# Kernel optimization log

Measured on AMD Instinct MI355X. Metric: run time of the kernel, lower is better.

## Reference

```python
import jax, jax.numpy as jnp
import numpy as np

NEG_INF = -1e9  # matches masked_fill value -1000000000.0
LEAKY_SLOPE = 0.2


def setup_inputs() -> dict:
    key = jax.random.key(0)
    k1, k2, k3, k4 = jax.random.split(key, 4)
    B, N, D_in, D_out = 8, 2048, 256, 256
    x = jax.random.normal(k1, (B, N, D_in), dtype=jnp.float32)
    adj_matrix = jax.random.randint(k2, (B, N, N), 0, 2, dtype=jnp.int32)
    # torch nn.Linear weights: W is [out, in], attention a is [1, 2*out]
    W = jax.random.normal(k3, (D_out, D_in), dtype=jnp.float32) / np.sqrt(D_in)
    a = jax.random.normal(k4, (1, 2 * D_out), dtype=jnp.float32) / np.sqrt(2 * D_out)
    return {"x": x, "adj_matrix": adj_matrix, "W": W, "a": a}


def reference(x, adj_matrix, W, a):
    # h = W(x): [B, N, D_out]
    h = jnp.einsum('bnd,od->bno', x, W)
    D = h.shape[-1]
    # attention(concat(h_i, h_j)) == h_i @ a_left + h_j @ a_right (bias-free linear)
    a_left, a_right = a[0, :D], a[0, D:]
    e = (h @ a_left)[:, :, None] + (h @ a_right)[:, None, :]  # [B, N, N]
    e = jnp.where(e > 0, e, LEAKY_SLOPE * e)  # LeakyReLU(0.2)
    e = jnp.where(adj_matrix == 0, NEG_INF, e)
    alpha = jax.nn.softmax(e, axis=-1)
    return jnp.einsum('bij,bjd->bid', alpha, h)
```

## Files before the change

kernel.cpp:

```cpp
#include <hip/hip_runtime.h>
#include <hip/hip_bf16.h>

typedef __attribute__((ext_vector_type(8))) __bf16 bf16x8;
typedef __attribute__((ext_vector_type(4))) float f32x4;
typedef __attribute__((ext_vector_type(4))) int int4v;

#define NB 8
#define NN 2048
#define ND 256
#define L2E 1.44269504f
#define AS1 __attribute__((address_space(1)))
#define AS3 __attribute__((address_space(3)))

__global__ __launch_bounds__(256) void k2_elr(
    const float* __restrict__ x, const float* __restrict__ W,
    const float* __restrict__ a, float* __restrict__ elc,
    float* __restrict__ er2) {
  __shared__ float wls[ND], wrs[ND];
  int t = threadIdx.x;
  {
    float swl = 0.f, swr = 0.f;
    for (int o = 0; o < ND; ++o) {
      float wv = W[(long)o * ND + t];
      swl = fmaf(a[o], wv, swl);
      swr = fmaf(a[ND + o], wv, swr);
    }
    wls[t] = swl;
    wrs[t] = swr;
  }
  __syncthreads();
  int r = t >> 2, q = t & 3;
  long row = (long)blockIdx.x * 64 + r;
  const f32x4* xr = (const f32x4*)(x + row * ND);
  float sl = 0.f, sr = 0.f;
#pragma unroll
  for (int ii = 0; ii < 16; ++ii) {
    int idx = q + (ii << 2);
    f32x4 xv = xr[idx];
    f32x4 lv = *(const f32x4*)(wls + idx * 4);
    f32x4 rv = *(const f32x4*)(wrs + idx * 4);
    sl += xv[0] * lv[0] + xv[1] * lv[1] + xv[2] * lv[2] + xv[3] * lv[3];
    sr += xv[0] * rv[0] + xv[1] * rv[1] + xv[2] * rv[2] + xv[3] * rv[3];
  }
  sl += __shfl_xor(sl, 1);
  sl += __shfl_xor(sl, 2);
  sr += __shfl_xor(sr, 1);
  sr += __shfl_xor(sr, 2);
  if (q == 0) {
    elc[row] = (-0.8f * sl - 16.0f) * L2E;
    float2 v;
    v.x = (sr - 16.0f) * L2E;
    v.y = 0.2f * sr * L2E;
    *(float2*)(er2 + row * 2) = v;
  }
}

__global__ __launch_bounds__(256) void k1_h(
    const float* __restrict__ x, const float* __restrict__ W,
    __bf16* __restrict__ hT2) {
  __shared__ __bf16 hlds[256 * 34];
  int tid = threadIdx.x;
  int wid = tid >> 6, lane = tid & 63;
  int msub = wid & 1, nh = wid >> 1;
  int lrow = lane & 15, kg = lane >> 4;
  int m0 = blockIdx.x * 32;
  int row = m0 + msub * 16 + lrow;

  f32x4 acc[8];
#pragma unroll
  for (int f = 0; f < 8; ++f) acc[f] = (f32x4){0.f, 0.f, 0.f, 0.f};

#pragma unroll
  for (int k0 = 0; k0 < ND; k0 += 32) {
    int kk = k0 + kg * 8;
    const f32x4* xa = (const f32x4*)(x + (long)row * ND + kk);
    f32x4 a0 = xa[0], a1 = xa[1];
    bf16x8 afrag;
    afrag[0] = (__bf16)a0[0]; afrag[1] = (__bf16)a0[1];
    afrag[2] = (__bf16)a0[2]; afrag[3] = (__bf16)a0[3];
    afrag[4] = (__bf16)a1[0]; afrag[5] = (__bf16)a1[1];
    afrag[6] = (__bf16)a1[2]; afrag[7] = (__bf16)a1[3];
#pragma unroll
    for (int f = 0; f < 8; ++f) {
      int o = nh * 128 + f * 16 + lrow;
      const f32x4* wb = (const f32x4*)(W + (long)o * ND + kk);
      f32x4 b0 = wb[0], b1 = wb[1];
      bf16x8 bfrag;
      bfrag[0] = (__bf16)b0[0]; bfrag[1] = (__bf16)b0[1];
      bfrag[2] = (__bf16)b0[2]; bfrag[3] = (__bf16)b0[3];
      bfrag[4] = (__bf16)b1[0]; bfrag[5] = (__bf16)b1[1];
      bfrag[6] = (__bf16)b1[2]; bfrag[7] = (__bf16)b1[3];
      acc[f] = __builtin_amdgcn_mfma_f32_16x16x32_bf16(afrag, bfrag, acc[f], 0, 0, 0);
    }
  }

#pragma unroll
  for (int f = 0; f < 8; ++f) {
    int d = nh * 128 + f * 16 + lrow;
#pragma unroll
    for (int r = 0; r < 4; ++r) {
      int nloc = msub * 16 + kg * 4 + r;
      hlds[d * 34 + nloc] = (__bf16)acc[f][r];
    }
  }
  __syncthreads();
  {
    int b = m0 >> 11;
    int jc = (m0 & (NN - 1)) >> 5;
    const int* src = (const int*)(hlds + tid * 34);
    int tmp[16];
#pragma unroll
    for (int j = 0; j < 16; ++j) tmp[j] = src[j];
    __bf16* dst = hT2 + (((long)b * 64 + jc) * 256 + tid) * 32;
#pragma unroll
    for (int j = 0; j < 4; ++j)
      *(int4v*)(dst + j * 8) = *(int4v*)(tmp + j * 4);
  }
}

__global__ __launch_bounds__(512, 4) void k3_main(
    const int* __restrict__ adj, const __bf16* __restrict__ hT2,
    const float* __restrict__ elc, const float* __restrict__ er2,
    float* __restrict__ out) {
  __shared__ __bf16 hbuf[4][8192];
  __shared__ float er_lds[NN * 2];

  int blk = blockIdx.x;
  int b = blk & 7;
  int it = blk >> 3;
  int tid = threadIdx.x;
  int wid = tid >> 6, lane = tid & 63;
  int isub = wid & 1, dh = wid >> 1;
  int lrow = lane & 15, kg = lane >> 4;
  int irow = it * 32 + isub * 16 + lrow;

  const __bf16* hT2b = hT2 + (long)b * 64 * 8192;
  const int* adjrow = adj + ((long)b * NN + irow) * NN;
  const float* er2b = er2 + (long)b * NN * 2;
  float c1s = elc[b * NN + irow];
  int kg8 = kg * 8;

  __builtin_amdgcn_global_load_lds((const AS1 void*)(er2b + tid * 4),
                                   (AS3 void*)(er_lds + tid * 4), 16, 0, 0);
  __builtin_amdgcn_global_load_lds((const AS1 void*)(er2b + 2048 + tid * 4),
                                   (AS3 void*)(er_lds + 2048 + tid * 4), 16, 0, 0);

  int d0 = tid >> 2, slot = tid & 3;
  int jlog = slot ^ (d0 & 3) ^ ((d0 >> 2) & 3);
  const __bf16* sgbase = hT2b + d0 * 32 + jlog * 8;

  int slot_r = kg ^ (lrow & 3) ^ ((lrow >> 2) & 3);
  int hoff = (dh * 64 + lrow) * 64 + slot_r * 16;
  int d_base = dh * 64 + lrow;

  f32x4 acc[4];
#pragma unroll
  for (int f = 0; f < 4; ++f) acc[f] = (f32x4){0.f, 0.f, 0.f, 0.f};
  float den = 0.f;

  int4v aj0_0, aj1_0, aj0_1, aj1_1, aj0_2, aj1_2, aj0_3, aj1_3;

#define STAGEH(BI, TCV)                                                     \
  {                                                                         \
    const __bf16* s_ = sgbase + (long)(TCV)*8192;                           \
    __builtin_amdgcn_global_load_lds((const AS1 void*)(s_),                 \
                                     (AS3 void*)(&hbuf[BI][tid * 8]), 16, 0, 0); \
    __builtin_amdgcn_global_load_lds(                                       \
        (const AS1 void*)(s_ + 4096),                                       \
        (AS3 void*)(&hbuf[BI][4096 + tid * 8]), 16, 0, 0);                  \
  }

#define LOADADJ(S, TCV)                                                     \
  {                                                                         \
    const int* ap_ = adjrow + (TCV)*32 + kg8;                               \
    aj0_##S = *(const int4v*)(ap_);                                         \
    aj1_##S = *(const int4v*)(ap_ + 4);                                     \
  }

#define COMPUTE(BI, S, TCV)                                                 \
  {                                                                         \
    const float* ep_ = er_lds + ((TCV)*32 + kg8) * 2;                       \
    f32x4 e0 = *(const f32x4*)(ep_);                                        \
    f32x4 e1 = *(const f32x4*)(ep_ + 4);                                    \
    f32x4 e2 = *(const f32x4*)(ep_ + 8);                                    \
    f32x4 e3 = *(const f32x4*)(ep_ + 12);                                   \
    bf16x8 pfrag;                                                           \
    float ps = 0.f;                                                         \
    _Pragma("unroll") for (int e = 0; e < 8; ++e) {                         \
      f32x4 ev = (e < 2) ? e0 : (e < 4) ? e1 : (e < 6) ? e2 : e3;           \
      float x16 = ev[(e & 1) * 2];                                          \
      float x02 = ev[(e & 1) * 2 + 1];                                      \
      int aj = (e < 4) ? aj0_##S[e] : aj1_##S[e & 3];                       \
      float m = fmaxf(x16, x02 + c1s);                                      \
      float p = __builtin_amdgcn_exp2f(m);                                  \
      p = aj ? p : 0.0f;                                                    \
      ps += p;                                                              \
      pfrag[e] = (__bf16)p;                                                 \
    }                                                                       \
    den += ps;                                                              \
    const char* hb = (const char*)&hbuf[BI][0];                             \
    __builtin_amdgcn_s_setprio(1);                                          \
    _Pragma("unroll") for (int f = 0; f < 4; ++f) {                         \
      bf16x8 bfr = *(const bf16x8*)(hb + hoff + f * 1024);                  \
      acc[f] = __builtin_amdgcn_mfma_f32_16x16x32_bf16(pfrag, bfr, acc[f], 0, 0, 0); \
    }                                                                       \
    __builtin_amdgcn_s_setprio(0);                                          \
  }

#define WAITB(VMN)                                       \
  asm volatile("s_waitcnt vmcnt(" VMN ")" ::: "memory"); \
  __builtin_amdgcn_s_barrier();

  LOADADJ(0, 0); STAGEH(0, 0);
  LOADADJ(1, 1); STAGEH(1, 1);
  LOADADJ(2, 2); STAGEH(2, 2);

  for (int t4 = 0; t4 < 15; ++t4) {
    int tc = t4 * 4;
    WAITB("8"); STAGEH(3, tc + 3); LOADADJ(3, tc + 3); COMPUTE(0, 0, tc);
    WAITB("8"); STAGEH(0, tc + 4); LOADADJ(0, tc + 4); COMPUTE(1, 1, tc + 1);
    WAITB("8"); STAGEH(1, tc + 5); LOADADJ(1, tc + 5); COMPUTE(2, 2, tc + 2);
    WAITB("8"); STAGEH(2, tc + 6); LOADADJ(2, tc + 6); COMPUTE(3, 3, tc + 3);
  }
  WAITB("8"); STAGEH(3, 63); LOADADJ(3, 63); COMPUTE(0, 0, 60);
  WAITB("8"); COMPUTE(1, 1, 61);
  WAITB("4"); COMPUTE(2, 2, 62);
  WAITB("0"); COMPUTE(3, 3, 63);

#undef STAGEH
#undef LOADADJ
#undef COMPUTE
#undef WAITB

  den += __shfl_xor(den, 16);
  den += __shfl_xor(den, 32);
  float rdiv[4];
#pragma unroll
  for (int r = 0; r < 4; ++r) rdiv[r] = 1.0f / __shfl(den, kg * 4 + r);

  float* outb = out + ((long)b * NN + it * 32 + isub * 16) * ND;
#pragma unroll
  for (int f = 0; f < 4; ++f) {
    int dcol = d_base + f * 16;
#pragma unroll
    for (int r = 0; r < 4; ++r)
      outb[(long)(kg * 4 + r) * ND + dcol] = acc[f][r] * rdiv[r];
  }
}

extern "C" void kernel_launch(void* const* d_in, const int* in_sizes, int n_in,
                              void* d_out, int out_size, void* d_ws,
                              size_t ws_size, hipStream_t stream) {
  const float* x = (const float*)d_in[0];
  const int* adj = (const int*)d_in[1];
  const float* W = (const float*)d_in[2];
  const float* a = (const float*)d_in[3];
  float* out = (float*)d_out;

  char* ws = (char*)d_ws;
  const size_t base = 8u * 1024u * 1024u;
  __bf16* hT2 = (__bf16*)ws;
  float* elc = (float*)(ws + base);
  float* er2 = (float*)(ws + base + 65536u);

  k1_h<<<dim3(512), dim3(256), 0, stream>>>(x, W, hT2);
  k2_elr<<<dim3(256), dim3(256), 0, stream>>>(x, W, a, elc, er2);
  k3_main<<<dim3(512), dim3(512), 0, stream>>>(adj, hT2, elc, er2, out);
}
```

Before: 131.8 us.

## Pack adjacency into bitmask in a pre-pass and shrink main-loop staging

Adds a pre-pass kernel that turns the int32 adjacency matrix into 64-bit ballot bitmasks. The main kernel then loads each block's 32-row mask slice into LDS once instead of streaming int adjacency per tile. The main loop drops from four h buffers to three, with a simpler swizzle and wait counts. The pre-pass still reads the full 128MB adjacency, so the main kernel's saving is traded for an extra full pass plus a launch.

Measured after the change: 131.7 us. About the same (-0.1%).

```diff
diff --git a/kernel.cpp b/kernel.cpp
--- a/kernel.cpp
+++ b/kernel.cpp
@@ -11,6 +11,19 @@
 #define L2E 1.44269504f
 #define AS1 __attribute__((address_space(1)))
 #define AS3 __attribute__((address_space(3)))
+
+__global__ __launch_bounds__(256) void k5_pack(
+    const int* __restrict__ adj, unsigned long long* __restrict__ mask) {
+  const long NSEG = (long)NB * NN * (NN / 64);
+  int lane = threadIdx.x & 63;
+  long gw = (((long)blockIdx.x * 256 + threadIdx.x) >> 6);
+  long stride = ((long)gridDim.x * 256) >> 6;
+  for (long s = gw; s < NSEG; s += stride) {
+    int v = adj[s * 64 + lane];
+    unsigned long long m = __ballot(v != 0);
+    if (lane == 0) mask[s] = m;
+  }
+}
 
 __global__ __launch_bounds__(256) void k2_elr(
     const float* __restrict__ x, const float* __restrict__ W,
@@ -119,11 +132,12 @@
 }
 
 __global__ __launch_bounds__(512, 4) void k3_main(
-    const int* __restrict__ adj, const __bf16* __restrict__ hT2,
+    const unsigned* __restrict__ mask32, const __bf16* __restrict__ hT2,
     const float* __restrict__ elc, const float* __restrict__ er2,
     float* __restrict__ out) {
-  __shared__ __bf16 hbuf[4][8192];
+  __shared__ __bf16 hbuf[3][8192];
   __shared__ float er_lds[NN * 2];
+  __shared__ unsigned mask_lds[32 * 65];
 
   int blk = blockIdx.x;
   int b = blk & 7;
@@ -135,100 +149,97 @@
   int irow = it * 32 + isub * 16 + lrow;
 
   const __bf16* hT2b = hT2 + (long)b * 64 * 8192;
-  const int* adjrow = adj + ((long)b * NN + irow) * NN;
+  const unsigned* maskb = mask32 + ((long)b * NN + (long)it * 32) * 64;
   const float* er2b = er2 + (long)b * NN * 2;
   float c1s = elc[b * NN + irow];
   int kg8 = kg * 8;
 
+  int4v mw = *(const int4v*)(maskb + tid * 4);
   __builtin_amdgcn_global_load_lds((const AS1 void*)(er2b + tid * 4),
                                    (AS3 void*)(er_lds + tid * 4), 16, 0, 0);
   __builtin_amdgcn_global_load_lds((const AS1 void*)(er2b + 2048 + tid * 4),
                                    (AS3 void*)(er_lds + 2048 + tid * 4), 16, 0, 0);
 
   int d0 = tid >> 2, slot = tid & 3;
-  int jlog = slot ^ (d0 & 3) ^ ((d0 >> 2) & 3);
+  int jlog = slot ^ ((d0 >> 1) & 3);
   const __bf16* sgbase = hT2b + d0 * 32 + jlog * 8;
 
-  int slot_r = kg ^ (lrow & 3) ^ ((lrow >> 2) & 3);
-  int hoff = (dh * 64 + lrow) * 64 + slot_r * 16;
+#define STAGEH(BI, TCV)                                                      \
+  {                                                                          \
+    const __bf16* s_ = sgbase + (long)(TCV)*8192;                            \
+    __builtin_amdgcn_global_load_lds((const AS1 void*)(s_),                  \
+                                     (AS3 void*)(&hbuf[BI][tid * 8]), 16, 0, 0); \
+    __builtin_amdgcn_global_load_lds(                                        \
+        (const AS1 void*)(s_ + 4096),                                        \
+        (AS3 void*)(&hbuf[BI][4096 + tid * 8]), 16, 0, 0);                   \
+  }
+
+  STAGEH(0, 0);
+  STAGEH(1, 1);
+
+  asm volatile("s_waitcnt vmcnt(6)" ::: "memory");
+  {
+    int mrow = tid >> 4, mcol = (tid & 15) * 4;
+    *(int4v*)(mask_lds + mrow * 65 + mcol) = mw;
+  }
+  asm volatile("s_waitcnt lgkmcnt(0)" ::: "memory");
+  __builtin_amdgcn_s_barrier();
+
+  int hoff = (dh * 64 + lrow) * 64 + (kg ^ ((lrow >> 1) & 3)) * 16;
   int d_base = dh * 64 + lrow;
+  int mbase = (isub * 16 + lrow) * 65;
 
   f32x4 acc[4];
 #pragma unroll
   for (int f = 0; f < 4; ++f) acc[f] = (f32x4){0.f, 0.f, 0.f, 0.f};
   float den = 0.f;
 
-  int4v aj0_0, aj1_0, aj0_1, aj1_1, aj0_2, aj1_2, aj0_3, aj1_3;
-
-#define STAGEH(BI, TCV)                                                     \
-  {                                                                         \
-    const __bf16* s_ = sgbase + (long)(TCV)*8192;                           \
-    __builtin_amdgcn_global_load_lds((const AS1 void*)(s_),                 \
-                                     (AS3 void*)(&hbuf[BI][tid * 8]), 16, 0, 0); \
-    __builtin_amdgcn_global_load_lds(                                       \
-        (const AS1 void*)(s_ + 4096),                                       \
-        (AS3 void*)(&hbuf[BI][4096 + tid * 8]), 16, 0, 0);                  \
-  }
-
-#define LOADADJ(S, TCV)                                                     \
-  {                                                                         \
-    const int* ap_ = adjrow + (TCV)*32 + kg8;                               \
-    aj0_##S = *(const int4v*)(ap_);                                         \
-    aj1_##S = *(const int4v*)(ap_ + 4);                                     \
-  }
-
-#define COMPUTE(BI, S, TCV)                                                 \
-  {                                                                         \
-    const float* ep_ = er_lds + ((TCV)*32 + kg8) * 2;                       \
-    f32x4 e0 = *(const f32x4*)(ep_);                                        \
-    f32x4 e1 = *(const f32x4*)(ep_ + 4);                                    \
-    f32x4 e2 = *(const f32x4*)(ep_ + 8);                                    \
-    f32x4 e3 = *(const f32x4*)(ep_ + 12);                                   \
-    bf16x8 pfrag;                                                           \
-    float ps = 0.f;                                                         \
-    _Pragma("unroll") for (int e = 0; e < 8; ++e) {                         \
-      f32x4 ev = (e < 2) ? e0 : (e < 4) ? e1 : (e < 6) ? e2 : e3;           \
-      float x16 = ev[(e & 1) * 2];                                          \
-      float x02 = ev[(e & 1) * 2 + 1];                                      \
-      int aj = (e < 4) ? aj0_##S[e] : aj1_##S[e & 3];                       \
-      float m = fmaxf(x16, x02 + c1s);                                      \
-      float p = __builtin_amdgcn_exp2f(m);                                  \
-      p = aj ? p : 0.0f;                                                    \
-      ps += p;                                                              \
-      pfrag[e] = (__bf16)p;                                                 \
-    }                                                                       \
-    den += ps;                                                              \
-    const char* hb = (const char*)&hbuf[BI][0];                             \
-    __builtin_amdgcn_s_setprio(1);                                          \
-    _Pragma("unroll") for (int f = 0; f < 4; ++f) {                         \
-      bf16x8 bfr = *(const bf16x8*)(hb + hoff + f * 1024);                  \
+#define COMPUTE(BI, TCV)                                                     \
+  {                                                                          \
+    unsigned msh = mask_lds[mbase + (TCV)] >> kg8;                           \
+    const float* ep_ = er_lds + ((TCV)*32 + kg8) * 2;                        \
+    f32x4 e0 = *(const f32x4*)(ep_);                                         \
+    f32x4 e1 = *(const f32x4*)(ep_ + 4);                                     \
+    f32x4 e2 = *(const f32x4*)(ep_ + 8);                                     \
+    f32x4 e3 = *(const f32x4*)(ep_ + 12);                                    \
+    bf16x8 pfrag;                                                            \
+    float ps = 0.f;                                                          \
+    _Pragma("unroll") for (int e = 0; e < 8; ++e) {                          \
+      f32x4 ev = (e < 2) ? e0 : (e < 4) ? e1 : (e < 6) ? e2 : e3;            \
+      float x16 = ev[(e & 1) * 2];                                           \
+      float x02 = ev[(e & 1) * 2 + 1];                                       \
+      float m = fmaxf(x16, x02 + c1s);                                       \
+      float p = __builtin_amdgcn_exp2f(m);                                   \
+      p = ((msh >> e) & 1u) ? p : 0.0f;                                      \
+      ps += p;                                                               \
+      pfrag[e] = (__bf16)p;                                                  \
+    }                                                                        \
+    den += ps;                                                               \
+    const char* hb = (const char*)&hbuf[BI][0];                              \
+    __builtin_amdgcn_s_setprio(1);                                           \
+    _Pragma("unroll") for (int f = 0; f < 4; ++f) {                          \
+      bf16x8 bfr = *(const bf16x8*)(hb + hoff + f * 1024);                   \
       acc[f] = __builtin_amdgcn_mfma_f32_16x16x32_bf16(pfrag, bfr, acc[f], 0, 0, 0); \
-    }                                                                       \
-    __builtin_amdgcn_s_setprio(0);                                          \
+    }                                                                        \
+    __builtin_amdgcn_s_setprio(0);                                           \
   }
 
 #define WAITB(VMN)                                       \
   asm volatile("s_waitcnt vmcnt(" VMN ")" ::: "memory"); \
   __builtin_amdgcn_s_barrier();
 
-  LOADADJ(0, 0); STAGEH(0, 0);
-  LOADADJ(1, 1); STAGEH(1, 1);
-  LOADADJ(2, 2); STAGEH(2, 2);
-
-  for (int t4 = 0; t4 < 15; ++t4) {
-    int tc = t4 * 4;
-    WAITB("8"); STAGEH(3, tc + 3); LOADADJ(3, tc + 3); COMPUTE(0, 0, tc);
-    WAITB("8"); STAGEH(0, tc + 4); LOADADJ(0, tc + 4); COMPUTE(1, 1, tc + 1);
-    WAITB("8"); STAGEH(1, tc + 5); LOADADJ(1, tc + 5); COMPUTE(2, 2, tc + 2);
-    WAITB("8"); STAGEH(2, tc + 6); LOADADJ(2, tc + 6); COMPUTE(3, 3, tc + 3);
-  }
-  WAITB("8"); STAGEH(3, 63); LOADADJ(3, 63); COMPUTE(0, 0, 60);
-  WAITB("8"); COMPUTE(1, 1, 61);
-  WAITB("4"); COMPUTE(2, 2, 62);
-  WAITB("0"); COMPUTE(3, 3, 63);
+  for (int t3 = 0; t3 < 20; ++t3) {
+    int tc = t3 * 3;
+    WAITB("2"); STAGEH(2, tc + 2); COMPUTE(0, tc);
+    WAITB("2"); STAGEH(0, tc + 3); COMPUTE(1, tc + 1);
+    WAITB("2"); STAGEH(1, tc + 4); COMPUTE(2, tc + 2);
+  }
+  WAITB("2"); STAGEH(2, 62); COMPUTE(0, 60);
+  WAITB("2"); STAGEH(0, 63); COMPUTE(1, 61);
+  WAITB("2"); COMPUTE(2, 62);
+  WAITB("0"); COMPUTE(0, 63);
 
 #undef STAGEH
-#undef LOADADJ
 #undef COMPUTE
 #undef WAITB
 
@@ -262,8 +273,12 @@
   __bf16* hT2 = (__bf16*)ws;
   float* elc = (float*)(ws + base);
   float* er2 = (float*)(ws + base + 65536u);
-
+  unsigned long long* mask =
+      (unsigned long long*)(ws + base + 262144u);
+
+  k5_pack<<<dim3(2048), dim3(256), 0, stream>>>(adj, mask);
   k1_h<<<dim3(512), dim3(256), 0, stream>>>(x, W, hT2);
   k2_elr<<<dim3(256), dim3(256), 0, stream>>>(x, W, a, elc, er2);
-  k3_main<<<dim3(512), dim3(512), 0, stream>>>(adj, hT2, elc, er2, out);
-}
+  k3_main<<<dim3(512), dim3(512), 0, stream>>>((const unsigned*)mask, hT2, elc,
+                                               er2, out);
+}
```

## Compress adjacency to LDS bitmasks via ballot and reuse h fragments across rows

Applied to the files above, without the earlier changes.

The main kernel is restructured to 256 threads per block. Each wave now owns 64 output columns for all 32 rows, so every h fragment read from LDS feeds two MFMAs. Adjacency rows are loaded coalesced along j, turned into 64-bit masks with a wave ballot, and stored as bit masks in LDS, replacing the per-lane int4 adjacency registers. The second right-attention term is now recomputed with an FMA from the first, which halves the er array. The trade-offs are extra LDS traffic and barriers for the mask handoff, a deeper software pipeline, and more registers per thread for the doubled accumulators.

Measured after the change: 125.5 us. -4.8%, faster.

```diff
diff --git a/kernel.cpp b/kernel.cpp
--- a/kernel.cpp
+++ b/kernel.cpp
@@ -15,7 +15,7 @@
 __global__ __launch_bounds__(256) void k2_elr(
     const float* __restrict__ x, const float* __restrict__ W,
     const float* __restrict__ a, float* __restrict__ elc,
-    float* __restrict__ er2) {
+    float* __restrict__ erx) {
   __shared__ float wls[ND], wrs[ND];
   int t = threadIdx.x;
   {
@@ -48,10 +48,7 @@
   sr += __shfl_xor(sr, 2);
   if (q == 0) {
     elc[row] = (-0.8f * sl - 16.0f) * L2E;
-    float2 v;
-    v.x = (sr - 16.0f) * L2E;
-    v.y = 0.2f * sr * L2E;
-    *(float2*)(er2 + row * 2) = v;
+    erx[row] = (sr - 16.0f) * L2E;
   }
 }
 
@@ -118,133 +115,170 @@
   }
 }
 
-__global__ __launch_bounds__(512, 4) void k3_main(
+__global__ __launch_bounds__(256, 2) void k3_main(
     const int* __restrict__ adj, const __bf16* __restrict__ hT2,
-    const float* __restrict__ elc, const float* __restrict__ er2,
+    const float* __restrict__ elc, const float* __restrict__ erx,
     float* __restrict__ out) {
   __shared__ __bf16 hbuf[4][8192];
-  __shared__ float er_lds[NN * 2];
+  __shared__ float er_lds[NN];
+  __shared__ unsigned mask_lds[2048];
 
   int blk = blockIdx.x;
   int b = blk & 7;
   int it = blk >> 3;
   int tid = threadIdx.x;
   int wid = tid >> 6, lane = tid & 63;
-  int isub = wid & 1, dh = wid >> 1;
   int lrow = lane & 15, kg = lane >> 4;
-  int irow = it * 32 + isub * 16 + lrow;
+  int kg8 = kg * 8;
 
   const __bf16* hT2b = hT2 + (long)b * 64 * 8192;
-  const int* adjrow = adj + ((long)b * NN + irow) * NN;
-  const float* er2b = er2 + (long)b * NN * 2;
-  float c1s = elc[b * NN + irow];
-  int kg8 = kg * 8;
-
-  __builtin_amdgcn_global_load_lds((const AS1 void*)(er2b + tid * 4),
+  const int* adjb = adj + ((long)b * NN + (long)it * 32) * NN;
+  const int* adjw = adjb + (long)wid * 8 * NN;
+  const float* erxb = erx + (long)b * NN;
+
+  float c1s0 = elc[b * NN + it * 32 + lrow];
+  float c1s1 = elc[b * NN + it * 32 + 16 + lrow];
+
+  __builtin_amdgcn_global_load_lds((const AS1 void*)(erxb + tid * 4),
                                    (AS3 void*)(er_lds + tid * 4), 16, 0, 0);
-  __builtin_amdgcn_global_load_lds((const AS1 void*)(er2b + 2048 + tid * 4),
-                                   (AS3 void*)(er_lds + 2048 + tid * 4), 16, 0, 0);
+  __builtin_amdgcn_global_load_lds((const AS1 void*)(erxb + 1024 + tid * 4),
+                                   (AS3 void*)(er_lds + 1024 + tid * 4), 16, 0, 0);
 
   int d0 = tid >> 2, slot = tid & 3;
-  int jlog = slot ^ (d0 & 3) ^ ((d0 >> 2) & 3);
+  int jlog = slot ^ ((tid >> 3) & 3);
   const __bf16* sgbase = hT2b + d0 * 32 + jlog * 8;
 
-  int slot_r = kg ^ (lrow & 3) ^ ((lrow >> 2) & 3);
-  int hoff = (dh * 64 + lrow) * 64 + slot_r * 16;
-  int d_base = dh * 64 + lrow;
-
-  f32x4 acc[4];
-#pragma unroll
-  for (int f = 0; f < 4; ++f) acc[f] = (f32x4){0.f, 0.f, 0.f, 0.f};
-  float den = 0.f;
-
-  int4v aj0_0, aj1_0, aj0_1, aj1_1, aj0_2, aj1_2, aj0_3, aj1_3;
-
-#define STAGEH(BI, TCV)                                                     \
-  {                                                                         \
-    const __bf16* s_ = sgbase + (long)(TCV)*8192;                           \
-    __builtin_amdgcn_global_load_lds((const AS1 void*)(s_),                 \
-                                     (AS3 void*)(&hbuf[BI][tid * 8]), 16, 0, 0); \
-    __builtin_amdgcn_global_load_lds(                                       \
-        (const AS1 void*)(s_ + 4096),                                       \
-        (AS3 void*)(&hbuf[BI][4096 + tid * 8]), 16, 0, 0);                  \
-  }
-
-#define LOADADJ(S, TCV)                                                     \
-  {                                                                         \
-    const int* ap_ = adjrow + (TCV)*32 + kg8;                               \
-    aj0_##S = *(const int4v*)(ap_);                                         \
-    aj1_##S = *(const int4v*)(ap_ + 4);                                     \
-  }
-
-#define COMPUTE(BI, S, TCV)                                                 \
-  {                                                                         \
-    const float* ep_ = er_lds + ((TCV)*32 + kg8) * 2;                       \
-    f32x4 e0 = *(const f32x4*)(ep_);                                        \
-    f32x4 e1 = *(const f32x4*)(ep_ + 4);                                    \
-    f32x4 e2 = *(const f32x4*)(ep_ + 8);                                    \
-    f32x4 e3 = *(const f32x4*)(ep_ + 12);                                   \
-    bf16x8 pfrag;                                                           \
-    float ps = 0.f;                                                         \
-    _Pragma("unroll") for (int e = 0; e < 8; ++e) {                         \
-      f32x4 ev = (e < 2) ? e0 : (e < 4) ? e1 : (e < 6) ? e2 : e3;           \
-      float x16 = ev[(e & 1) * 2];                                          \
-      float x02 = ev[(e & 1) * 2 + 1];                                      \
-      int aj = (e < 4) ? aj0_##S[e] : aj1_##S[e & 3];                       \
-      float m = fmaxf(x16, x02 + c1s);                                      \
-      float p = __builtin_amdgcn_exp2f(m);                                  \
-      p = aj ? p : 0.0f;                                                    \
-      ps += p;                                                              \
-      pfrag[e] = (__bf16)p;                                                 \
-    }                                                                       \
-    den += ps;                                                              \
-    const char* hb = (const char*)&hbuf[BI][0];                             \
-    __builtin_amdgcn_s_setprio(1);                                          \
-    _Pragma("unroll") for (int f = 0; f < 4; ++f) {                         \
-      bf16x8 bfr = *(const bf16x8*)(hb + hoff + f * 1024);                  \
-      acc[f] = __builtin_amdgcn_mfma_f32_16x16x32_bf16(pfrag, bfr, acc[f], 0, 0, 0); \
-    }                                                                       \
-    __builtin_amdgcn_s_setprio(0);                                          \
-  }
-
-#define WAITB(VMN)                                       \
-  asm volatile("s_waitcnt vmcnt(" VMN ")" ::: "memory"); \
+  int hoff = (wid * 64 + lrow) * 64 + (kg ^ ((lrow >> 1) & 3)) * 16;
+
+  f32x4 acc[2][4];
+#pragma unroll
+  for (int g = 0; g < 2; ++g)
+#pragma unroll
+    for (int f = 0; f < 4; ++f) acc[g][f] = (f32x4){0.f, 0.f, 0.f, 0.f};
+  float den0 = 0.f, den1 = 0.f;
+
+  int av0[4], av1[4];
+
+#define STAGEH(BI, TCV)                                                       \
+  {                                                                           \
+    const __bf16* s_ = sgbase + (long)(TCV)*8192;                             \
+    _Pragma("unroll") for (int rr = 0; rr < 4; ++rr) {                        \
+      __builtin_amdgcn_global_load_lds(                                       \
+          (const AS1 void*)(s_ + rr * 2048),                                  \
+          (AS3 void*)(&hbuf[BI][(rr * 256 + tid) * 8]), 16, 0, 0);            \
+    }                                                                         \
+  }
+
+#define ADJLOAD(S, P, H)                                                      \
+  {                                                                           \
+    const int* ap_ = adjw + (long)(H)*4 * NN + (long)(P)*64 + lane;           \
+    _Pragma("unroll") for (int i = 0; i < 4; ++i)                             \
+        av##S[i] = ap_[(long)i * NN];                                         \
+  }
+
+#define BALLOT(S, P, H)                                                       \
+  {                                                                           \
+    _Pragma("unroll") for (int i = 0; i < 4; ++i) {                           \
+      unsigned long long mb_ = __ballot(av##S[i] != 0);                       \
+      int R_ = wid * 8 + (H)*4 + i;                                           \
+      if (lane == 0) {                                                        \
+        mask_lds[R_ * 64 + ((2 * (P)) ^ (R_ & 31))] = (unsigned)mb_;          \
+        mask_lds[R_ * 64 + ((2 * (P) + 1) ^ (R_ & 31))] = (unsigned)(mb_ >> 32); \
+      }                                                                       \
+    }                                                                         \
+  }
+
+#define COMPUTE(BI, TCV)                                                      \
+  {                                                                           \
+    unsigned msh0 = mask_lds[lrow * 64 + ((TCV) ^ lrow)] >> kg8;              \
+    unsigned msh1 = mask_lds[(lrow + 16) * 64 + ((TCV) ^ lrow ^ 16)] >> kg8;  \
+    const float* ep_ = er_lds + (TCV)*32 + kg8;                               \
+    f32x4 x16a = *(const f32x4*)(ep_);                                        \
+    f32x4 x16b = *(const f32x4*)(ep_ + 4);                                    \
+    bf16x8 pf0, pf1;                                                          \
+    float ps0 = 0.f, ps1 = 0.f;                                               \
+    _Pragma("unroll") for (int e = 0; e < 8; ++e) {                           \
+      float x16 = (e < 4) ? x16a[e] : x16b[e - 4];                            \
+      float x02 = fmaf(0.2f, x16, 4.61662413f);                               \
+      float m0_ = fmaxf(x16, x02 + c1s0);                                     \
+      float m1_ = fmaxf(x16, x02 + c1s1);                                     \
+      float p0 = __builtin_amdgcn_exp2f(m0_);                                 \
+      float p1 = __builtin_amdgcn_exp2f(m1_);                                 \
+      p0 = ((msh0 >> e) & 1u) ? p0 : 0.0f;                                    \
+      p1 = ((msh1 >> e) & 1u) ? p1 : 0.0f;                                    \
+      ps0 += p0; ps1 += p1;                                                   \
+      pf0[e] = (__bf16)p0; pf1[e] = (__bf16)p1;                               \
+    }                                                                         \
+    den0 += ps0; den1 += ps1;                                                 \
+    const char* hb_ = (const char*)&hbuf[BI][0];                              \
+    __builtin_amdgcn_s_setprio(1);                                            \
+    _Pragma("unroll") for (int f = 0; f < 4; ++f) {                           \
+      bf16x8 bfr = *(const bf16x8*)(hb_ + hoff + f * 1024);                   \
+      acc[0][f] = __builtin_amdgcn_mfma_f32_16x16x32_bf16(pf0, bfr, acc[0][f], 0, 0, 0); \
+      acc[1][f] = __builtin_amdgcn_mfma_f32_16x16x32_bf16(pf1, bfr, acc[1][f], 0, 0, 0); \
+    }                                                                         \
+    __builtin_amdgcn_s_setprio(0);                                            \
+  }
+
+#define WAITX(VMN)                                                        \
+  asm volatile("s_waitcnt vmcnt(" VMN ") lgkmcnt(0)" ::: "memory");       \
   __builtin_amdgcn_s_barrier();
 
-  LOADADJ(0, 0); STAGEH(0, 0);
-  LOADADJ(1, 1); STAGEH(1, 1);
-  LOADADJ(2, 2); STAGEH(2, 2);
-
-  for (int t4 = 0; t4 < 15; ++t4) {
-    int tc = t4 * 4;
-    WAITB("8"); STAGEH(3, tc + 3); LOADADJ(3, tc + 3); COMPUTE(0, 0, tc);
-    WAITB("8"); STAGEH(0, tc + 4); LOADADJ(0, tc + 4); COMPUTE(1, 1, tc + 1);
-    WAITB("8"); STAGEH(1, tc + 5); LOADADJ(1, tc + 5); COMPUTE(2, 2, tc + 2);
-    WAITB("8"); STAGEH(2, tc + 6); LOADADJ(2, tc + 6); COMPUTE(3, 3, tc + 3);
-  }
-  WAITB("8"); STAGEH(3, 63); LOADADJ(3, 63); COMPUTE(0, 0, 60);
-  WAITB("8"); COMPUTE(1, 1, 61);
-  WAITB("4"); COMPUTE(2, 2, 62);
-  WAITB("0"); COMPUTE(3, 3, 63);
+  STAGEH(0, 0);
+  STAGEH(1, 1);
+  ADJLOAD(0, 0, 0);
+  ADJLOAD(1, 0, 1);
+  asm volatile("s_waitcnt vmcnt(0)" ::: "memory");
+  BALLOT(0, 0, 0);
+  BALLOT(1, 0, 1);
+  ADJLOAD(0, 1, 0);
+  ADJLOAD(1, 1, 1);
+  asm volatile("s_waitcnt lgkmcnt(0)" ::: "memory");
+  __builtin_amdgcn_s_barrier();
+
+  for (int T = 0; T < 15; ++T) {
+    int tc = T * 4;
+    WAITX("8"); STAGEH(2, tc + 2); BALLOT(0, (tc >> 1) + 1, 0);
+    ADJLOAD(0, (tc >> 1) + 2, 0); COMPUTE(0, tc);
+    WAITX("8"); STAGEH(3, tc + 3); BALLOT(1, (tc >> 1) + 1, 1);
+    ADJLOAD(1, (tc >> 1) + 2, 1); COMPUTE(1, tc + 1);
+    WAITX("8"); STAGEH(0, tc + 4); BALLOT(0, (tc >> 1) + 2, 0);
+    ADJLOAD(0, (tc >> 1) + 3, 0); COMPUTE(2, tc + 2);
+    WAITX("8"); STAGEH(1, tc + 5); BALLOT(1, (tc >> 1) + 2, 1);
+    ADJLOAD(1, (tc >> 1) + 3, 1); COMPUTE(3, tc + 3);
+  }
+  WAITX("8"); STAGEH(2, 62); BALLOT(0, 31, 0); COMPUTE(0, 60);
+  WAITX("4"); STAGEH(3, 63); BALLOT(1, 31, 1); COMPUTE(1, 61);
+  WAITX("4"); COMPUTE(2, 62);
+  WAITX("0"); COMPUTE(3, 63);
 
 #undef STAGEH
-#undef LOADADJ
+#undef ADJLOAD
+#undef BALLOT
 #undef COMPUTE
-#undef WAITB
-
-  den += __shfl_xor(den, 16);
-  den += __shfl_xor(den, 32);
-  float rdiv[4];
-#pragma unroll
-  for (int r = 0; r < 4; ++r) rdiv[r] = 1.0f / __shfl(den, kg * 4 + r);
-
-  float* outb = out + ((long)b * NN + it * 32 + isub * 16) * ND;
+#undef WAITX
+
+  den0 += __shfl_xor(den0, 16);
+  den0 += __shfl_xor(den0, 32);
+  den1 += __shfl_xor(den1, 16);
+  den1 += __shfl_xor(den1, 32);
+  float rdiv0[4], rdiv1[4];
+#pragma unroll
+  for (int r = 0; r < 4; ++r) {
+    rdiv0[r] = 1.0f / __shfl(den0, kg * 4 + r);
+    rdiv1[r] = 1.0f / __shfl(den1, kg * 4 + r);
+  }
+
+  float* outb = out + ((long)b * NN + (long)it * 32) * ND;
 #pragma unroll
   for (int f = 0; f < 4; ++f) {
-    int dcol = d_base + f * 16;
-#pragma unroll
-    for (int r = 0; r < 4; ++r)
-      outb[(long)(kg * 4 + r) * ND + dcol] = acc[f][r] * rdiv[r];
+    int dcol = wid * 64 + f * 16 + lrow;
+#pragma unroll
+    for (int r = 0; r < 4; ++r) {
+      int rr = kg * 4 + r;
+      outb[(long)rr * ND + dcol] = acc[0][f][r] * rdiv0[r];
+      outb[(long)(16 + rr) * ND + dcol] = acc[1][f][r] * rdiv1[r];
+    }
   }
 }
 
@@ -261,9 +295,9 @@
   const size_t base = 8u * 1024u * 1024u;
   __bf16* hT2 = (__bf16*)ws;
   float* elc = (float*)(ws + base);
-  float* er2 = (float*)(ws + base + 65536u);
+  float* erx = (float*)(ws + base + 65536u);
 
   k1_h<<<dim3(512), dim3(256), 0, stream>>>(x, W, hT2);
-  k2_elr<<<dim3(256), dim3(256), 0, stream>>>(x, W, a, elc, er2);
-  k3_main<<<dim3(512), dim3(512), 0, stream>>>(adj, hT2, elc, er2, out);
+  k2_elr<<<dim3(256), dim3(256), 0, stream>>>(x, W, a, elc, erx);
+  k3_main<<<dim3(512), dim3(256), 0, stream>>>(adj, hT2, elc, erx, out);
 }
```
